# Kernel tuning notes

Hardware: AMD Instinct MI355X
Metric: run time of the kernel (lower is better)

Reference implementation:

```python
import jax, jax.numpy as jnp
import numpy as np

NUM_FIELDS = 16
EMBED = 32
W1 = 7
W2 = 5
VOCAB = 100000
BATCH = 4096
K1 = NUM_FIELDS // 2  # first k-max pool size (num_inputs/2)
K2 = 3                # second k-max pool size
DN = ('NHWC', 'HWIO', 'NHWC')


def kmax_pool_last(x, k):
    # k-max pooling along the last axis (tf.nn.top_k values)
    return jax.lax.top_k(x, k)[0]


def setup_inputs() -> dict:
    key = jax.random.key(0)
    ks = jax.random.split(key, 6)
    return {
        'idx': jax.random.randint(ks[0], (BATCH, NUM_FIELDS), 0, VOCAB),
        'w0': jax.random.normal(ks[1], (NUM_FIELDS, VOCAB, EMBED), jnp.float32) * 0.02,
        'b0': jnp.zeros((NUM_FIELDS, EMBED), jnp.float32),
        'f1': jax.random.normal(ks[2], (EMBED, W1, 1, 2), jnp.float32) * 0.1,
        'f2': jax.random.normal(ks[3], (EMBED, W2, 2, 2), jnp.float32) * 0.1,
        'w1': jax.random.normal(ks[4], (2 * 3 * EMBED, 1), jnp.float32) * 0.02,
        'b1': jnp.zeros((1,), jnp.float32),
    }


def reference(idx, w0, b0, f1, f2, w1, b1):
    # sparse one-hot matmul == embedding row gather: [B, F, E]
    emb = w0[jnp.arange(NUM_FIELDS)[None, :], idx] + b0[None, :, :]
    l = jnp.tanh(emb)  # layer_acts[0] = tanh; dropout identity at test
    # reshape [-1, F, E, 1] then transpose [0,2,1,3] -> [B, E, F, 1]
    l = jnp.transpose(l[..., None], (0, 2, 1, 3))
    # conv1: kernel [E, W1, 1, 2], SAME -> [B, E, F, 2]
    l = jax.lax.conv_general_dilated(l, f1, (1, 1), 'SAME', dimension_numbers=DN)
    # k-max pool over field axis (last axis after transpose) -> [B, E, K1, 2]
    l = jnp.transpose(kmax_pool_last(jnp.transpose(l, (0, 1, 3, 2)), K1), (0, 1, 3, 2))
    # conv2: kernel [E, W2, 2, 2], SAME -> [B, E, K1, 2]
    l = jax.lax.conv_general_dilated(l, f2, (1, 1), 'SAME', dimension_numbers=DN)
    # second k-max pool -> [B, E, 3, 2]
    l = jnp.transpose(kmax_pool_last(jnp.transpose(l, (0, 1, 3, 2)), K2), (0, 1, 3, 2))
    l = jnp.tanh(l.reshape(l.shape[0], EMBED * 3 * 2))  # layer_acts[1] = tanh
    logits = (l @ w1 + b1).reshape(-1)  # layer_acts[2] = none
    return jax.nn.sigmoid(logits)  # y_prob
```

## Files before the change

### kernel.cpp

```cpp
#include <hip/hip_runtime.h>
#include <math.h>

#define NF 16
#define EMB 32
#define VOCAB 100000
#define TS 28
#define NROW 63
#define C1STR 36

__device__ __forceinline__ float tanhf_fast(float x) {
    float e = __expf(2.f * x);
    return 1.f - 2.f * __builtin_amdgcn_rcpf(e + 1.f);
}

__global__ __launch_bounds__(64) void ccpm_fwd(
    const int* __restrict__ idx,
    const float* __restrict__ w0,
    const float* __restrict__ b0,
    const float* __restrict__ f1,
    const float* __restrict__ f2,
    const float* __restrict__ w1,
    const float* __restrict__ b1,
    float* __restrict__ out)
{
    const int b = blockIdx.x;
    const int l = threadIdx.x;

    __shared__ float buf[NROW * TS];
    __shared__ float c1s[32 * C1STR];
    float* c2s = c1s;

    const float4 z4 = make_float4(0.f, 0.f, 0.f, 0.f);

    for (int i = l; i < (NROW * TS) / 4; i += 64) ((float4*)buf)[i] = z4;
    __syncthreads();

    {
        int f  = l >> 2;
        int e0 = (l & 3) * 8;
        int row = idx[b * NF + f];
        const float* src  = w0 + ((size_t)f * VOCAB + row) * EMB + e0;
        const float* bsrc = b0 + f * EMB + e0;
        float4 v0 = ((const float4*)src)[0];
        float4 v1 = ((const float4*)src)[1];
        float4 u0 = ((const float4*)bsrc)[0];
        float4 u1 = ((const float4*)bsrc)[1];
        float g[8];
        g[0]=v0.x+u0.x; g[1]=v0.y+u0.y; g[2]=v0.z+u0.z; g[3]=v0.w+u0.w;
        g[4]=v1.x+u1.x; g[5]=v1.y+u1.y; g[6]=v1.z+u1.z; g[7]=v1.w+u1.w;
        #pragma unroll
        for (int i = 0; i < 8; ++i)
            buf[(e0 + i + 15) * TS + f + 3] = tanhf_fast(g[i]);
    }
    __syncthreads();

    const int h  = l >> 1;
    const int wh = l & 1;

    {
        const int wb = wh * 8;
        float a0[8], a1[8];
        #pragma unroll
        for (int w = 0; w < 8; ++w) { a0[w] = 0.f; a1[w] = 0.f; }
        const float2* f1v = (const float2*)f1;
        for (int kh = 0; kh < 32; ++kh) {
            const float* r = &buf[(h + kh) * TS + wb];
            float4 q0 = ((const float4*)r)[0];
            float4 q1 = ((const float4*)r)[1];
            float4 q2 = ((const float4*)r)[2];
            float4 q3 = ((const float4*)r)[3];
            float win[16];
            win[0]=q0.x; win[1]=q0.y; win[2]=q0.z; win[3]=q0.w;
            win[4]=q1.x; win[5]=q1.y; win[6]=q1.z; win[7]=q1.w;
            win[8]=q2.x; win[9]=q2.y; win[10]=q2.z; win[11]=q2.w;
            win[12]=q3.x; win[13]=q3.y; win[14]=q3.z; win[15]=q3.w;
            #pragma unroll
            for (int kw = 0; kw < 7; ++kw) {
                float2 fp = f1v[kh * 7 + kw];
                #pragma unroll
                for (int w = 0; w < 8; ++w) {
                    a0[w] += win[w + kw] * fp.x;
                    a1[w] += win[w + kw] * fp.y;
                }
            }
        }
        float* crow = &c1s[h * C1STR + wb];
        ((float4*)crow)[0] = make_float4(a0[0], a0[1], a0[2], a0[3]);
        ((float4*)crow)[1] = make_float4(a0[4], a0[5], a0[6], a0[7]);
        ((float4*)(crow + 16))[0] = make_float4(a1[0], a1[1], a1[2], a1[3]);
        ((float4*)(crow + 16))[1] = make_float4(a1[4], a1[5], a1[6], a1[7]);
    }
    __syncthreads();

    for (int i = l; i < (NROW * TS) / 4; i += 64) ((float4*)buf)[i] = z4;
    __syncthreads();

    {
        int e = h, o = wh;
        const float* row = &c1s[e * C1STR + o * 16];
        float4 q0 = ((const float4*)row)[0];
        float4 q1 = ((const float4*)row)[1];
        float4 q2 = ((const float4*)row)[2];
        float4 q3 = ((const float4*)row)[3];
        float v[16];
        v[0]=q0.x; v[1]=q0.y; v[2]=q0.z; v[3]=q0.w;
        v[4]=q1.x; v[5]=q1.y; v[6]=q1.z; v[7]=q1.w;
        v[8]=q2.x; v[9]=q2.y; v[10]=q2.z; v[11]=q2.w;
        v[12]=q3.x; v[13]=q3.y; v[14]=q3.z; v[15]=q3.w;
        #pragma unroll
        for (int i = 0; i < 16; ++i) {
            int r = 0;
            #pragma unroll
            for (int j = 0; j < 16; ++j) {
                if (j == i) continue;
                r += ((v[j] > v[i]) || (v[j] == v[i] && j < i)) ? 1 : 0;
            }
            if (r < 8) buf[(e + 15) * TS + o * 12 + 2 + r] = v[i];
        }
    }
    __syncthreads();

    {
        const int wb = wh * 4;
        float a0[4], a1[4];
        #pragma unroll
        for (int w = 0; w < 4; ++w) { a0[w] = 0.f; a1[w] = 0.f; }
        const float4* f2q = (const float4*)f2;
        for (int kh = 0; kh < 32; ++kh) {
            const float* r = &buf[(h + kh) * TS];
            float4 p0a = ((const float4*)(r + wb))[0];
            float4 p0b = ((const float4*)(r + wb))[1];
            float4 p1a = ((const float4*)(r + 12 + wb))[0];
            float4 p1b = ((const float4*)(r + 12 + wb))[1];
            float q0[8], q1[8];
            q0[0]=p0a.x; q0[1]=p0a.y; q0[2]=p0a.z; q0[3]=p0a.w;
            q0[4]=p0b.x; q0[5]=p0b.y; q0[6]=p0b.z; q0[7]=p0b.w;
            q1[0]=p1a.x; q1[1]=p1a.y; q1[2]=p1a.z; q1[3]=p1a.w;
            q1[4]=p1b.x; q1[5]=p1b.y; q1[6]=p1b.z; q1[7]=p1b.w;
            #pragma unroll
            for (int kw = 0; kw < 5; ++kw) {
                float4 fp = f2q[kh * 5 + kw];
                #pragma unroll
                for (int w = 0; w < 4; ++w) {
                    a0[w] += q0[w + kw] * fp.x + q1[w + kw] * fp.z;
                    a1[w] += q0[w + kw] * fp.y + q1[w + kw] * fp.w;
                }
            }
        }
        float* crow = &c2s[h * 16 + wb];
        ((float4*)crow)[0]       = make_float4(a0[0], a0[1], a0[2], a0[3]);
        ((float4*)(crow + 8))[0] = make_float4(a1[0], a1[1], a1[2], a1[3]);
    }
    __syncthreads();

    {
        int e = h, o = wh;
        const float* row = &c2s[e * 16 + o * 8];
        float4 qa = ((const float4*)row)[0];
        float4 qb = ((const float4*)row)[1];
        float v[8];
        v[0]=qa.x; v[1]=qa.y; v[2]=qa.z; v[3]=qa.w;
        v[4]=qb.x; v[5]=qb.y; v[6]=qb.z; v[7]=qb.w;
        float t0 = 0.f, t1 = 0.f, t2 = 0.f;
        #pragma unroll
        for (int i = 0; i < 8; ++i) {
            int r = 0;
            #pragma unroll
            for (int j = 0; j < 8; ++j) {
                if (j == i) continue;
                r += ((v[j] > v[i]) || (v[j] == v[i] && j < i)) ? 1 : 0;
            }
            t0 = (r == 0) ? v[i] : t0;
            t1 = (r == 1) ? v[i] : t1;
            t2 = (r == 2) ? v[i] : t2;
        }
        float s = tanhf_fast(t0) * w1[e * 6 + o]
                + tanhf_fast(t1) * w1[e * 6 + 2 + o]
                + tanhf_fast(t2) * w1[e * 6 + 4 + o];
        #pragma unroll
        for (int off = 32; off; off >>= 1) s += __shfl_xor(s, off, 64);
        if (l == 0) {
            float logit = s + b1[0];
            out[b] = __builtin_amdgcn_rcpf(1.f + __expf(-logit));
        }
    }
}

extern "C" void kernel_launch(void* const* d_in, const int* in_sizes, int n_in,
                              void* d_out, int out_size, void* d_ws, size_t ws_size,
                              hipStream_t stream) {
    const int*   idx = (const int*)d_in[0];
    const float* w0  = (const float*)d_in[1];
    const float* b0  = (const float*)d_in[2];
    const float* f1  = (const float*)d_in[3];
    const float* f2  = (const float*)d_in[4];
    const float* w1  = (const float*)d_in[5];
    const float* b1  = (const float*)d_in[6];
    float* out = (float*)d_out;
    ccpm_fwd<<<out_size, 64, 0, stream>>>(idx, w0, b0, f1, f2, w1, b1, out);
}
```

Baseline: 310.5 us.

## Store conv activations in fp16 LDS and exchange k-max data via lane shuffles

The shared staging buffer now holds fp16 instead of fp32, halving LDS footprint and read traffic per conv window. The conv1 and conv2 outputs stay in registers and are swapped between lane pairs with __shfl_xor before the k-max selection, which removes the separate c1s/c2s shared arrays and one barrier. Ranking switches to pairwise comparisons that update both ranks at once, which halves the compare count. Launch bounds request higher occupancy and the kh loops are unrolled by two. The fp16 rounding of activations may change results slightly and could reorder near-tied values in top-k.

New measurement: 294.4 us. 1.05x faster.

```diff
diff --git a/kernel.cpp b/kernel.cpp
--- a/kernel.cpp
+++ b/kernel.cpp
@@ -2,18 +2,19 @@
 #include <math.h>
 
 #define NF 16
-#define EMB 32
 #define VOCAB 100000
-#define TS 28
+#define TSH 40
 #define NROW 63
-#define C1STR 36
+
+typedef _Float16 half8 __attribute__((ext_vector_type(8)));
+typedef _Float16 half4 __attribute__((ext_vector_type(4)));
 
 __device__ __forceinline__ float tanhf_fast(float x) {
     float e = __expf(2.f * x);
     return 1.f - 2.f * __builtin_amdgcn_rcpf(e + 1.f);
 }
 
-__global__ __launch_bounds__(64) void ccpm_fwd(
+__global__ __launch_bounds__(64, 6) void ccpm_fwd(
     const int* __restrict__ idx,
     const float* __restrict__ w0,
     const float* __restrict__ b0,
@@ -26,54 +27,51 @@
     const int b = blockIdx.x;
     const int l = threadIdx.x;
 
-    __shared__ float buf[NROW * TS];
-    __shared__ float c1s[32 * C1STR];
-    float* c2s = c1s;
+    __shared__ __align__(16) _Float16 buf[NROW * TSH + 8];
 
     const float4 z4 = make_float4(0.f, 0.f, 0.f, 0.f);
-
-    for (int i = l; i < (NROW * TS) / 4; i += 64) ((float4*)buf)[i] = z4;
+    float4* bz = (float4*)buf;
+
+    #pragma unroll
+    for (int i = 0; i < 5; ++i) {
+        int n = i * 64 + l;
+        if (n < (NROW * TSH + 8) / 8) bz[n] = z4;
+    }
     __syncthreads();
 
     {
         int f  = l >> 2;
         int e0 = (l & 3) * 8;
         int row = idx[b * NF + f];
-        const float* src  = w0 + ((size_t)f * VOCAB + row) * EMB + e0;
-        const float* bsrc = b0 + f * EMB + e0;
-        float4 v0 = ((const float4*)src)[0];
-        float4 v1 = ((const float4*)src)[1];
-        float4 u0 = ((const float4*)bsrc)[0];
-        float4 u1 = ((const float4*)bsrc)[1];
+        const float4* src = (const float4*)(w0 + ((size_t)f * VOCAB + row) * 32 + e0);
+        const float4* bb  = (const float4*)(b0 + f * 32 + e0);
+        float4 v0 = src[0], v1 = src[1];
+        float4 u0 = bb[0],  u1 = bb[1];
         float g[8];
         g[0]=v0.x+u0.x; g[1]=v0.y+u0.y; g[2]=v0.z+u0.z; g[3]=v0.w+u0.w;
         g[4]=v1.x+u1.x; g[5]=v1.y+u1.y; g[6]=v1.z+u1.z; g[7]=v1.w+u1.w;
         #pragma unroll
         for (int i = 0; i < 8; ++i)
-            buf[(e0 + i + 15) * TS + f + 3] = tanhf_fast(g[i]);
+            buf[(e0 + i + 15) * TSH + f + 3] = (_Float16)tanhf_fast(g[i]);
     }
     __syncthreads();
 
     const int h  = l >> 1;
     const int wh = l & 1;
 
-    {
-        const int wb = wh * 8;
-        float a0[8], a1[8];
+    float a0[8], a1[8];
+    {
         #pragma unroll
         for (int w = 0; w < 8; ++w) { a0[w] = 0.f; a1[w] = 0.f; }
         const float2* f1v = (const float2*)f1;
+        #pragma unroll 2
         for (int kh = 0; kh < 32; ++kh) {
-            const float* r = &buf[(h + kh) * TS + wb];
-            float4 q0 = ((const float4*)r)[0];
-            float4 q1 = ((const float4*)r)[1];
-            float4 q2 = ((const float4*)r)[2];
-            float4 q3 = ((const float4*)r)[3];
+            const half8* r = (const half8*)&buf[(h + kh) * TSH + 8 * wh];
+            half8 wa = r[0];
+            half8 wbv = r[1];
             float win[16];
-            win[0]=q0.x; win[1]=q0.y; win[2]=q0.z; win[3]=q0.w;
-            win[4]=q1.x; win[5]=q1.y; win[6]=q1.z; win[7]=q1.w;
-            win[8]=q2.x; win[9]=q2.y; win[10]=q2.z; win[11]=q2.w;
-            win[12]=q3.x; win[13]=q3.y; win[14]=q3.z; win[15]=q3.w;
+            #pragma unroll
+            for (int i = 0; i < 8; ++i) { win[i] = (float)wa[i]; win[8 + i] = (float)wbv[i]; }
             #pragma unroll
             for (int kw = 0; kw < 7; ++kw) {
                 float2 fp = f1v[kh * 7 + kw];
@@ -84,99 +82,110 @@
                 }
             }
         }
-        float* crow = &c1s[h * C1STR + wb];
-        ((float4*)crow)[0] = make_float4(a0[0], a0[1], a0[2], a0[3]);
-        ((float4*)crow)[1] = make_float4(a0[4], a0[5], a0[6], a0[7]);
-        ((float4*)(crow + 16))[0] = make_float4(a1[0], a1[1], a1[2], a1[3]);
-        ((float4*)(crow + 16))[1] = make_float4(a1[4], a1[5], a1[6], a1[7]);
-    }
-    __syncthreads();
-
-    for (int i = l; i < (NROW * TS) / 4; i += 64) ((float4*)buf)[i] = z4;
-    __syncthreads();
-
-    {
-        int e = h, o = wh;
-        const float* row = &c1s[e * C1STR + o * 16];
-        float4 q0 = ((const float4*)row)[0];
-        float4 q1 = ((const float4*)row)[1];
-        float4 q2 = ((const float4*)row)[2];
-        float4 q3 = ((const float4*)row)[3];
+    }
+    __syncthreads();
+
+    #pragma unroll
+    for (int i = 0; i < 5; ++i) {
+        int n = i * 64 + l;
+        if (n < (NROW * TSH + 8) / 8) bz[n] = z4;
+    }
+    __syncthreads();
+
+    {
+        float own[8], recv[8];
+        #pragma unroll
+        for (int i = 0; i < 8; ++i) {
+            own[i]  = wh ? a1[i] : a0[i];
+            recv[i] = __shfl_xor(wh ? a0[i] : a1[i], 1, 64);
+        }
         float v[16];
-        v[0]=q0.x; v[1]=q0.y; v[2]=q0.z; v[3]=q0.w;
-        v[4]=q1.x; v[5]=q1.y; v[6]=q1.z; v[7]=q1.w;
-        v[8]=q2.x; v[9]=q2.y; v[10]=q2.z; v[11]=q2.w;
-        v[12]=q3.x; v[13]=q3.y; v[14]=q3.z; v[15]=q3.w;
-        #pragma unroll
-        for (int i = 0; i < 16; ++i) {
-            int r = 0;
-            #pragma unroll
-            for (int j = 0; j < 16; ++j) {
-                if (j == i) continue;
-                r += ((v[j] > v[i]) || (v[j] == v[i] && j < i)) ? 1 : 0;
-            }
-            if (r < 8) buf[(e + 15) * TS + o * 12 + 2 + r] = v[i];
-        }
-    }
-    __syncthreads();
-
-    {
-        const int wb = wh * 4;
-        float a0[4], a1[4];
-        #pragma unroll
-        for (int w = 0; w < 4; ++w) { a0[w] = 0.f; a1[w] = 0.f; }
+        #pragma unroll
+        for (int i = 0; i < 8; ++i) {
+            v[i]     = wh ? recv[i] : own[i];
+            v[8 + i] = wh ? own[i] : recv[i];
+        }
+        int r[16];
+        #pragma unroll
+        for (int i = 0; i < 16; ++i) r[i] = 0;
+        #pragma unroll
+        for (int i = 0; i < 16; ++i)
+            #pragma unroll
+            for (int j = i + 1; j < 16; ++j) {
+                bool ge = v[i] >= v[j];
+                r[j] += ge ? 1 : 0;
+                r[i] += ge ? 0 : 1;
+            }
+        #pragma unroll
+        for (int i = 0; i < 16; ++i)
+            if (r[i] < 8) buf[(h + 15) * TSH + wh * 12 + 2 + r[i]] = (_Float16)v[i];
+    }
+    __syncthreads();
+
+    float c0[4], c1[4];
+    {
+        #pragma unroll
+        for (int w = 0; w < 4; ++w) { c0[w] = 0.f; c1[w] = 0.f; }
         const float4* f2q = (const float4*)f2;
+        #pragma unroll 2
         for (int kh = 0; kh < 32; ++kh) {
-            const float* r = &buf[(h + kh) * TS];
-            float4 p0a = ((const float4*)(r + wb))[0];
-            float4 p0b = ((const float4*)(r + wb))[1];
-            float4 p1a = ((const float4*)(r + 12 + wb))[0];
-            float4 p1b = ((const float4*)(r + 12 + wb))[1];
+            const _Float16* rw = &buf[(h + kh) * TSH];
+            half4 p0a = *(const half4*)(rw + 4 * wh);
+            half4 p0b = *(const half4*)(rw + 4 * wh + 4);
+            half4 p1a = *(const half4*)(rw + 12 + 4 * wh);
+            half4 p1b = *(const half4*)(rw + 16 + 4 * wh);
             float q0[8], q1[8];
-            q0[0]=p0a.x; q0[1]=p0a.y; q0[2]=p0a.z; q0[3]=p0a.w;
-            q0[4]=p0b.x; q0[5]=p0b.y; q0[6]=p0b.z; q0[7]=p0b.w;
-            q1[0]=p1a.x; q1[1]=p1a.y; q1[2]=p1a.z; q1[3]=p1a.w;
-            q1[4]=p1b.x; q1[5]=p1b.y; q1[6]=p1b.z; q1[7]=p1b.w;
+            #pragma unroll
+            for (int i = 0; i < 4; ++i) {
+                q0[i] = (float)p0a[i]; q0[4 + i] = (float)p0b[i];
+                q1[i] = (float)p1a[i]; q1[4 + i] = (float)p1b[i];
+            }
             #pragma unroll
             for (int kw = 0; kw < 5; ++kw) {
                 float4 fp = f2q[kh * 5 + kw];
                 #pragma unroll
                 for (int w = 0; w < 4; ++w) {
-                    a0[w] += q0[w + kw] * fp.x + q1[w + kw] * fp.z;
-                    a1[w] += q0[w + kw] * fp.y + q1[w + kw] * fp.w;
+                    c0[w] += q0[w + kw] * fp.x + q1[w + kw] * fp.z;
+                    c1[w] += q0[w + kw] * fp.y + q1[w + kw] * fp.w;
                 }
             }
         }
-        float* crow = &c2s[h * 16 + wb];
-        ((float4*)crow)[0]       = make_float4(a0[0], a0[1], a0[2], a0[3]);
-        ((float4*)(crow + 8))[0] = make_float4(a1[0], a1[1], a1[2], a1[3]);
-    }
-    __syncthreads();
-
-    {
-        int e = h, o = wh;
-        const float* row = &c2s[e * 16 + o * 8];
-        float4 qa = ((const float4*)row)[0];
-        float4 qb = ((const float4*)row)[1];
+    }
+
+    {
+        float own[4], recv[4];
+        #pragma unroll
+        for (int i = 0; i < 4; ++i) {
+            own[i]  = wh ? c1[i] : c0[i];
+            recv[i] = __shfl_xor(wh ? c0[i] : c1[i], 1, 64);
+        }
         float v[8];
-        v[0]=qa.x; v[1]=qa.y; v[2]=qa.z; v[3]=qa.w;
-        v[4]=qb.x; v[5]=qb.y; v[6]=qb.z; v[7]=qb.w;
+        #pragma unroll
+        for (int i = 0; i < 4; ++i) {
+            v[i]     = wh ? recv[i] : own[i];
+            v[4 + i] = wh ? own[i] : recv[i];
+        }
+        int r[8];
+        #pragma unroll
+        for (int i = 0; i < 8; ++i) r[i] = 0;
+        #pragma unroll
+        for (int i = 0; i < 8; ++i)
+            #pragma unroll
+            for (int j = i + 1; j < 8; ++j) {
+                bool ge = v[i] >= v[j];
+                r[j] += ge ? 1 : 0;
+                r[i] += ge ? 0 : 1;
+            }
         float t0 = 0.f, t1 = 0.f, t2 = 0.f;
         #pragma unroll
         for (int i = 0; i < 8; ++i) {
-            int r = 0;
-            #pragma unroll
-            for (int j = 0; j < 8; ++j) {
-                if (j == i) continue;
-                r += ((v[j] > v[i]) || (v[j] == v[i] && j < i)) ? 1 : 0;
-            }
-            t0 = (r == 0) ? v[i] : t0;
-            t1 = (r == 1) ? v[i] : t1;
-            t2 = (r == 2) ? v[i] : t2;
-        }
-        float s = tanhf_fast(t0) * w1[e * 6 + o]
-                + tanhf_fast(t1) * w1[e * 6 + 2 + o]
-                + tanhf_fast(t2) * w1[e * 6 + 4 + o];
+            t0 = (r[i] == 0) ? v[i] : t0;
+            t1 = (r[i] == 1) ? v[i] : t1;
+            t2 = (r[i] == 2) ? v[i] : t2;
+        }
+        float s = tanhf_fast(t0) * w1[h * 6 + wh]
+                + tanhf_fast(t1) * w1[h * 6 + 2 + wh]
+                + tanhf_fast(t2) * w1[h * 6 + 4 + wh];
         #pragma unroll
         for (int off = 32; off; off >>= 1) s += __shfl_xor(s, off, 64);
         if (l == 0) {
```
